# Performance work log

Hardware: AMD Instinct MI355X
Metric: run time of the kernel (lower is better)

The kernel has to match this reference:

```python
import jax, jax.numpy as jnp
import numpy as np

B, S, DM, TD, H, HD = 2, 2048, 1024, 1024, 16, 64


def setup_inputs() -> dict:
    key = jax.random.key(0)
    k1, k2, k3, k4 = jax.random.split(key, 4)
    query = jax.random.normal(k1, (B, S, DM), dtype=jnp.float32)
    # fused QKV projection weight (nn.Linear weight layout: [out, in]) and output proj
    W_in = jax.random.normal(k2, (3 * TD, DM), dtype=jnp.float32) * 0.02
    W_out = jax.random.normal(k3, (DM, TD), dtype=jnp.float32) * 0.02
    # standard RoPE tables, broadcastable against [B, H, S, HD]
    inv_freq = 1.0 / (10000.0 ** (jnp.arange(0, HD, 2, dtype=jnp.float32) / HD))
    t = jnp.arange(S, dtype=jnp.float32)
    freqs = jnp.outer(t, inv_freq)                      # [S, HD/2]
    emb = jnp.concatenate([freqs, freqs], axis=-1)      # [S, HD]
    sin_q = jnp.sin(emb)[None, None]                    # [1,1,S,HD]
    cos_q = jnp.cos(emb)[None, None]
    # padding mask over keys: first length[b] positions valid (>= S/2 so no NaN rows)
    lengths = jax.random.randint(k4, (B,), S // 2, S + 1)
    attn_mask = jnp.arange(S)[None, :] < lengths[:, None]  # [B, S] bool
    return {"query": query, "W_in": W_in, "W_out": W_out,
            "sin_q": sin_q, "cos_q": cos_q, "attn_mask": attn_mask}


def _rotate_half(x):
    x1, x2 = jnp.split(x, 2, axis=-1)
    return jnp.concatenate([-x2, x1], axis=-1)


def reference(query, W_in, W_out, sin_q, cos_q, attn_mask):
    # fused QKV projection (proj_in, bias=False)
    qkv = query @ W_in.T                                # [B, S, 3*TD]
    q, k, v = jnp.split(qkv, 3, axis=-1)
    to_heads = lambda x: x.reshape(B, S, H, HD).transpose(0, 2, 1, 3)  # [B,H,S,HD]
    q, k, v = to_heads(q), to_heads(k), to_heads(v)
    # RoPE (prefix = 0 since sin covers full sequence)
    q = q * cos_q + _rotate_half(q) * sin_q
    k = k * cos_q + _rotate_half(k) * sin_q
    # SDPA with padding-mask bias + causal mask
    scale = 1.0 / jnp.sqrt(jnp.float32(HD))
    scores = jnp.einsum('bhqd,bhkd->bhqk', q, k) * scale  # [B,H,S,S]
    causal = jnp.arange(S)[:, None] >= jnp.arange(S)[None, :]  # [S, S]
    mask = attn_mask[:, None, None, :] & causal[None, None]    # [B,1,S,S]
    scores = jnp.where(mask, scores, -jnp.inf)
    attn = jax.nn.softmax(scores, axis=-1)
    out = jnp.einsum('bhqk,bhkd->bhqd', attn, v)        # [B,H,S,HD]
    out = out.transpose(0, 2, 1, 3).reshape(B, S, TD)
    return out @ W_out.T                                 # [B, S, DM]
```

## Files before the change

kernel.cpp:

```cpp
#include <hip/hip_runtime.h>
#include <hip/hip_bf16.h>

#define B_ 2
#define S_ 2048
#define DM_ 1024
#define TD_ 1024
#define H_ 16
#define HD_ 64

using bf16 = __hip_bfloat16;
typedef __attribute__((ext_vector_type(8))) short s8v;
typedef __attribute__((ext_vector_type(4))) float f4v;

__device__ __forceinline__ f4v mfma_bf16(s8v a, s8v b, f4v c) {
    return __builtin_amdgcn_mfma_f32_16x16x32_bf16(a, b, c, 0, 0, 0);
}

__device__ __forceinline__ unsigned cvt_pk_bf16(float a, float b) {
    unsigned r;
    asm("v_cvt_pk_bf16_f32 %0, %1, %2" : "=v"(r) : "v"(a), "v"(b));
    return r;
}
__device__ __forceinline__ int2 pack4bf(float a, float b, float c, float d) {
    int2 r;
    r.x = (int)cvt_pk_bf16(a, b);
    r.y = (int)cvt_pk_bf16(c, d);
    return r;
}

__device__ __forceinline__ bool detect_f32(const unsigned int* __restrict__ cosw) {
    return (cosw[0] & 0xFFFFu) == 0u;
}

__device__ __forceinline__ void gload_lds16(const bf16* g, void* l) {
    __builtin_amdgcn_global_load_lds(
        (const __attribute__((address_space(1))) unsigned int*)(const void*)g,
        (__attribute__((address_space(3))) unsigned int*)l,
        16, 0, 0);
}

#define NQ_  (B_ * S_ * DM_)
#define NWI_ (3 * TD_ * DM_)
#define NWO_ (DM_ * TD_)
#define NCVT_BLOCKS ((NQ_ + NWI_ + NWO_) / 2048)

__global__ __launch_bounds__(256)
void prep_all(const void* __restrict__ q, const void* __restrict__ wi,
              const void* __restrict__ wo, bf16* __restrict__ dst,
              const void* __restrict__ mask, int* __restrict__ lengths,
              const unsigned int* __restrict__ cosw) {
    const int bid = blockIdx.x;
    if (bid < NCVT_BLOCKS) {
        const bool f32 = detect_f32(cosw);
        int i = (bid * 256 + threadIdx.x) * 8;
        const void* src; int off;
        if (i < NQ_)              { src = q;  off = i; }
        else if (i < NQ_ + NWI_)  { src = wi; off = i - NQ_; }
        else                      { src = wo; off = i - NQ_ - NWI_; }
        if (f32) {
            const float* p = (const float*)src + off;
            float4 x = *reinterpret_cast<const float4*>(p);
            float4 y = *reinterpret_cast<const float4*>(p + 4);
            union { unsigned u[4]; int4 v; } t;
            t.u[0] = cvt_pk_bf16(x.x, x.y);
            t.u[1] = cvt_pk_bf16(x.z, x.w);
            t.u[2] = cvt_pk_bf16(y.x, y.y);
            t.u[3] = cvt_pk_bf16(y.z, y.w);
            *reinterpret_cast<int4*>(dst + i) = t.v;
        } else {
            *reinterpret_cast<int4*>(dst + i) =
                *reinterpret_cast<const int4*>((const bf16*)src + off);
        }
        return;
    }
    int b = bid - NCVT_BLOCKS;
    unsigned int w0 = ((const unsigned int*)mask)[0];
    int enc;
    if (w0 == 1u) enc = 0;
    else if (w0 == 0x01010101u) enc = 1;
    else if (w0 == 0x3F803F80u) enc = 2;
    else enc = 3;
    int cnt = 0;
    for (int s = threadIdx.x; s < S_; s += 256) {
        int i = b * S_ + s;
        bool v;
        if (enc == 0)      v = ((const int*)mask)[i] != 0;
        else if (enc == 1) v = ((const unsigned char*)mask)[i] != 0;
        else if (enc == 2) v = ((const unsigned short*)mask)[i] != 0;
        else               v = ((const float*)mask)[i] != 0.f;
        cnt += v ? 1 : 0;
    }
    __shared__ int red[256];
    red[threadIdx.x] = cnt;
    __syncthreads();
    for (int off = 128; off > 0; off >>= 1) {
        if (threadIdx.x < off) red[threadIdx.x] += red[threadIdx.x + off];
        __syncthreads();
    }
    if (threadIdx.x == 0) lengths[b] = red[0];
}

__global__ __launch_bounds__(256, 4)
void gemm_out(const bf16* __restrict__ A, const bf16* __restrict__ Bm,
              void* __restrict__ C, int M, int N, int K,
              int c_dyn, const unsigned int* __restrict__ cosw) {
    __shared__ bf16 lds_a[128 * 64];
    __shared__ bf16 lds_b[64 * 64];

    const bool cf32 = c_dyn && detect_f32(cosw);

    const int t = threadIdx.x;
    const int wave = t >> 6, lane = t & 63;
    const int quad = lane >> 4, l16 = lane & 15;
    const int wm = wave >> 1, wn = wave & 1;
    const int bid = blockIdx.x;
    const int c = bid & 7, g = bid >> 3;
    const int m0 = (c * 4 + (g & 3)) * 128;
    const int n0 = (g >> 2) * 64;
    const int wuni = __builtin_amdgcn_readfirstlane(wave);

    f4v acc[4][2];
    #pragma unroll
    for (int i = 0; i < 4; i++)
        #pragma unroll
        for (int j = 0; j < 2; j++)
            acc[i][j] = f4v{0.f, 0.f, 0.f, 0.f};

    for (int k0 = 0; k0 < K; k0 += 64) {
        __syncthreads();
        #pragma unroll
        for (int i = 0; i < 4; i++) {
            int ci = i * 256 + t;
            int row = ci >> 3;
            int csrc = (ci & 7) ^ (row & 7);
            gload_lds16(A + (size_t)(m0 + row) * K + k0 + csrc * 8,
                        (char*)lds_a + i * 4096 + wuni * 1024);
        }
        #pragma unroll
        for (int i = 0; i < 2; i++) {
            int ci = i * 256 + t;
            int row = ci >> 3;
            int csrc = (ci & 7) ^ (row & 7);
            gload_lds16(Bm + (size_t)(n0 + row) * K + k0 + csrc * 8,
                        (char*)lds_b + i * 4096 + wuni * 1024);
        }
        __syncthreads();

        #pragma unroll
        for (int kk = 0; kk < 2; kk++) {
            s8v afr[4], bfr[2];
            #pragma unroll
            for (int mb = 0; mb < 4; mb++) {
                int r = wm * 64 + mb * 16 + l16;
                int ch = (kk * 4 + quad) ^ (l16 & 7);
                afr[mb] = *reinterpret_cast<const s8v*>(&lds_a[r * 64 + ch * 8]);
            }
            #pragma unroll
            for (int nb = 0; nb < 2; nb++) {
                int r = wn * 32 + nb * 16 + l16;
                int ch = (kk * 4 + quad) ^ (l16 & 7);
                bfr[nb] = *reinterpret_cast<const s8v*>(&lds_b[r * 64 + ch * 8]);
            }
            #pragma unroll
            for (int mb = 0; mb < 4; mb++)
                #pragma unroll
                for (int nb = 0; nb < 2; nb++)
                    acc[mb][nb] = mfma_bf16(bfr[nb], afr[mb], acc[mb][nb]);
        }
    }

    #pragma unroll
    for (int mb = 0; mb < 4; mb++) {
        int m = m0 + wm * 64 + mb * 16 + l16;
        #pragma unroll
        for (int nb = 0; nb < 2; nb++) {
            int n = n0 + wn * 32 + nb * 16 + quad * 4;
            f4v v = acc[mb][nb];
            if (cf32) {
                *reinterpret_cast<f4v*>(&((float*)C)[(size_t)m * N + n]) = v;
            } else {
                *reinterpret_cast<int2*>(&((bf16*)C)[(size_t)m * N + n]) =
                    pack4bf(v[0], v[1], v[2], v[3]);
            }
        }
    }
}

__global__ __launch_bounds__(256, 3)
void gemm_qkv(const bf16* __restrict__ A, const bf16* __restrict__ Bm,
              bf16* __restrict__ Qh, bf16* __restrict__ Kt, bf16* __restrict__ Vt,
              const void* __restrict__ sin_t, const void* __restrict__ cos_t) {
    __shared__ bf16 lds_a[128 * 64];
    __shared__ bf16 lds_b[128 * 64];

    const int t = threadIdx.x;
    const int wave = t >> 6, lane = t & 63;
    const int quad = lane >> 4, l16 = lane & 15;
    const int wm = wave >> 1, wn = wave & 1;
    const int bid = blockIdx.x;
    const int c = bid & 7, g = bid >> 3;
    const int m0 = (c * 4 + (g & 3)) * 128;
    const int n0 = (g >> 2) * 128;
    const int wuni = __builtin_amdgcn_readfirstlane(wave);

    f4v acc[4][4];
    #pragma unroll
    for (int i = 0; i < 4; i++)
        #pragma unroll
        for (int j = 0; j < 4; j++)
            acc[i][j] = f4v{0.f, 0.f, 0.f, 0.f};

    for (int k0 = 0; k0 < 1024; k0 += 64) {
        __syncthreads();
        #pragma unroll
        for (int i = 0; i < 4; i++) {
            int ci = i * 256 + t;
            int row = ci >> 3;
            int csrc = (ci & 7) ^ (row & 7);
            gload_lds16(A + (size_t)(m0 + row) * 1024 + k0 + csrc * 8,
                        (char*)lds_a + i * 4096 + wuni * 1024);
            gload_lds16(Bm + (size_t)(n0 + row) * 1024 + k0 + csrc * 8,
                        (char*)lds_b + i * 4096 + wuni * 1024);
        }
        __syncthreads();

        #pragma unroll
        for (int kk = 0; kk < 2; kk++) {
            s8v afr[4], bfr[4];
            #pragma unroll
            for (int mb = 0; mb < 4; mb++) {
                int r = wm * 64 + mb * 16 + l16;
                int ch = (kk * 4 + quad) ^ (l16 & 7);
                afr[mb] = *reinterpret_cast<const s8v*>(&lds_a[r * 64 + ch * 8]);
            }
            #pragma unroll
            for (int nb = 0; nb < 4; nb++) {
                int r = wn * 64 + nb * 16 + l16;
                int ch = (kk * 4 + quad) ^ (l16 & 7);
                bfr[nb] = *reinterpret_cast<const s8v*>(&lds_b[r * 64 + ch * 8]);
            }
            #pragma unroll
            for (int mb = 0; mb < 4; mb++)
                #pragma unroll
                for (int nb = 0; nb < 4; nb++)
                    acc[mb][nb] = mfma_bf16(bfr[nb], afr[mb], acc[mb][nb]);
        }
    }

    const int region = n0 >> 10;
    if (region < 2) {
        const bool f32 = detect_f32((const unsigned int*)cos_t);
        #pragma unroll
        for (int mb = 0; mb < 4; mb++) {
            const int m = m0 + wm * 64 + mb * 16 + l16;
            const int b = m >> 11, s = m & 2047;
            #pragma unroll
            for (int nb = 0; nb < 4; nb++) {
                const int n = n0 + wn * 64 + nb * 16 + quad * 4;
                const int d = n & 63;
                const int h = (n >> 6) & 15;
                const float sgn = (nb < 2) ? -1.f : 1.f;
                f4v v  = acc[mb][nb];
                f4v vp = acc[mb][nb ^ 2];
                float cs[4], sn[4];
                if (f32) {
                    float4 c4 = *reinterpret_cast<const float4*>(
                        (const float*)cos_t + s * 64 + d);
                    float4 s4 = *reinterpret_cast<const float4*>(
                        (const float*)sin_t + s * 64 + d);
                    cs[0] = c4.x; cs[1] = c4.y; cs[2] = c4.z; cs[3] = c4.w;
                    sn[0] = s4.x; sn[1] = s4.y; sn[2] = s4.z; sn[3] = s4.w;
                } else {
                    const bf16* cp = (const bf16*)cos_t + s * 64 + d;
                    const bf16* sp = (const bf16*)sin_t + s * 64 + d;
                    #pragma unroll
                    for (int r = 0; r < 4; r++) {
                        cs[r] = __bfloat162float(cp[r]);
                        sn[r] = __bfloat162float(sp[r]);
                    }
                }
                float y[4];
                #pragma unroll
                for (int r = 0; r < 4; r++)
                    y[r] = v[r] * cs[r] + sgn * vp[r] * sn[r];
                if (region == 0) {
                    size_t o = ((size_t)(b * H_ + h) * S_ + s) * 64 + d;
                    *reinterpret_cast<int2*>(&Qh[o]) =
                        pack4bf(y[0] * 0.180336880f, y[1] * 0.180336880f,
                                y[2] * 0.180336880f, y[3] * 0.180336880f);
                } else {
                    size_t kt = ((size_t)(b * H_ + h) * 32 + (s >> 6)) * 4096;
                    int dp = ((((d >> 3) ^ (s & 7)) << 3) | (d & 7));
                    *reinterpret_cast<int2*>(&Kt[kt + (s & 63) * 64 + dp]) =
                        pack4bf(y[0], y[1], y[2], y[3]);
                }
            }
        }
    } else {
        __syncthreads();
        bf16* half_w = (wm == 0) ? lds_a : lds_b;
        #pragma unroll
        for (int mb = 0; mb < 4; mb++) {
            const int slr = mb * 16 + l16;
            #pragma unroll
            for (int nb = 0; nb < 4; nb++) {
                const int nl = wn * 64 + nb * 16 + quad * 4;
                f4v v = acc[mb][nb];
                int off = (((nl >> 3) ^ (slr & 7)) << 3) | (nl & 7);
                *reinterpret_cast<int2*>(&half_w[slr * 128 + off]) =
                    pack4bf(v[0], v[1], v[2], v[3]);
            }
        }
        __syncthreads();
        const int b  = m0 >> 11;
        const int h0 = (n0 - 2048) >> 6;
        const int r0 = t & 7;
        #pragma unroll
        for (int i = 0; i < 8; i++) {
            int id  = i * 256 + t;
            int kc  = id & 7;
            int d   = (id >> 3) & 63;
            int sbl = (id >> 9) & 1;
            int hh  = id >> 10;
            int cb  = (hh << 3) | (d >> 3);
            const short* half_r = reinterpret_cast<const short*>(
                sbl ? lds_b : lds_a);
            union { short s_[8]; int4 v4; } u;
            #pragma unroll
            for (int j = 0; j < 8; j++) {
                int e   = (j + r0) & 7;
                int slr = kc * 8 + e;
                u.s_[e] = half_r[slr * 128 + (((cb ^ e) << 3) | (d & 7))];
            }
            size_t tb = ((size_t)(b * H_ + h0 + hh) * 32 +
                         ((m0 & 2047) >> 6) + sbl) * 4096;
            *reinterpret_cast<int4*>(&Vt[tb + d * 64 + ((kc ^ (d & 7)) << 3)]) = u.v4;
        }
    }
}

__global__ __launch_bounds__(256)
void attn_fused(const bf16* __restrict__ Qh, const bf16* __restrict__ Kt,
                const bf16* __restrict__ Vt, const int* __restrict__ lengths,
                bf16* __restrict__ out) {
    __shared__ bf16 k_buf[2 * 4096];
    __shared__ bf16 v_buf[2 * 4096];
    __shared__ bf16 lds_p[4 * 16 * 72];

    const int t = threadIdx.x, wave = t >> 6, lane = t & 63;
    const int quad = lane >> 4, l16 = lane & 15;
    const int bid = blockIdx.x;
    const int slot = bid >> 3;
    const int bh = (bid & 7) * 4 + (slot >> 4);
    const int p = slot & 15;
    const int b = bh >> 4, h = bh & 15;

    const size_t hb = (size_t)bh * S_ * 64;
    const bf16* Ktp = Kt + (size_t)bh * 32 * 4096;
    const bf16* Vtp = Vt + (size_t)bh * 32 * 4096;
    const int wuni = __builtin_amdgcn_readfirstlane(wave);
    int len_raw = lengths[b];
    const int len_b = len_raw < 1 ? 1 : (len_raw > S_ ? S_ : len_raw);
    const int nkt_len = (len_b + 63) >> 6;

    s8v ones;
    #pragma unroll
    for (int i = 0; i < 8; i++) ones[i] = (short)0x3F80;

    #pragma unroll
    for (int pass = 0; pass < 2; pass++) {
        const int qb = pass ? (31 - p) : p;
        const int qrow_g = qb * 64 + wave * 16 + l16;
        const int kmax = (qrow_g < len_b - 1) ? qrow_g : (len_b - 1);

        s8v qf[2];
        {
            const bf16* qptr = Qh + hb + (size_t)qrow_g * 64 + quad * 8;
            qf[0] = *reinterpret_cast<const s8v*>(qptr);
            qf[1] = *reinterpret_cast<const s8v*>(qptr + 32);
        }

        f4v o_acc[4];
        #pragma unroll
        for (int a = 0; a < 4; a++) o_acc[a] = f4v{0.f, 0.f, 0.f, 0.f};
        f4v l_acc = f4v{0.f, 0.f, 0.f, 0.f};

        const int nkt = (qb + 1) < nkt_len ? (qb + 1) : nkt_len;

        f4v s_prev[4];
        auto process_tile = [&](int pt, const bf16* vb) {
            const int pbase = pt * 64;
            const bool tail = (pt == qb) || (pbase + 64 > len_b);
            #pragma unroll
            for (int a = 0; a < 4; a++) {
                float e0[4];
                #pragma unroll
                for (int r = 0; r < 4; r++) {
                    float e = __builtin_amdgcn_exp2f(s_prev[a][r]);
                    if (tail) {
                        int key = pbase + a * 16 + quad * 4 + r;
                        e = (key <= kmax) ? e : 0.f;
                    }
                    e0[r] = e;
                }
                *reinterpret_cast<int2*>(
                    &lds_p[(wave * 16 + l16) * 72 + a * 16 + quad * 4]) =
                    pack4bf(e0[0], e0[1], e0[2], e0[3]);
            }
            asm volatile("s_waitcnt lgkmcnt(0)" ::: "memory");
            __builtin_amdgcn_s_setprio(1);
            #pragma unroll
            for (int kk = 0; kk < 2; kk++) {
                s8v pf = *reinterpret_cast<const s8v*>(
                    &lds_p[(wave * 16 + l16) * 72 + kk * 32 + quad * 8]);
                l_acc = mfma_bf16(ones, pf, l_acc);
                #pragma unroll
                for (int a = 0; a < 4; a++) {
                    int ch = (kk * 4 + quad) ^ (l16 & 7);
                    s8v vf = *reinterpret_cast<const s8v*>(
                        &vb[(a * 16 + l16) * 64 + ch * 8]);
                    o_acc[a] = mfma_bf16(vf, pf, o_acc[a]);
                }
            }
            __builtin_amdgcn_s_setprio(0);
        };

        #pragma unroll
        for (int i = 0; i < 2; i++) {
            int ci = i * 256 + t;
            gload_lds16(Ktp + ci * 8, (char*)k_buf + i * 4096 + wuni * 1024);
        }
        __syncthreads();

        for (int kt = 0; kt < nkt; kt++) {
            const int cur = kt & 1;
            {
                const bf16* vst = Vtp + (size_t)kt * 4096;
                #pragma unroll
                for (int i = 0; i < 2; i++) {
                    int ci = i * 256 + t;
                    gload_lds16(vst + ci * 8,
                                (char*)v_buf + cur * 8192 + i * 4096 + wuni * 1024);
                }
            }
            if (kt + 1 < nkt) {
                const bf16* kst = Ktp + (size_t)(kt + 1) * 4096;
                #pragma unroll
                for (int i = 0; i < 2; i++) {
                    int ci = i * 256 + t;
                    gload_lds16(kst + ci * 8,
                                (char*)k_buf + (cur ^ 1) * 8192 + i * 4096 + wuni * 1024);
                }
            }

            const bf16* kb = k_buf + cur * 4096;
            f4v s_acc[4];
            #pragma unroll
            for (int a = 0; a < 4; a++) s_acc[a] = f4v{0.f, 0.f, 0.f, 0.f};
            __builtin_amdgcn_s_setprio(1);
            #pragma unroll
            for (int kk = 0; kk < 2; kk++) {
                #pragma unroll
                for (int a = 0; a < 4; a++) {
                    int ch = (kk * 4 + quad) ^ (l16 & 7);
                    s8v kf = *reinterpret_cast<const s8v*>(
                        &kb[(a * 16 + l16) * 64 + ch * 8]);
                    s_acc[a] = mfma_bf16(kf, qf[kk], s_acc[a]);
                }
            }
            __builtin_amdgcn_s_setprio(0);

            if (kt > 0) process_tile(kt - 1, v_buf + ((kt - 1) & 1) * 4096);

            #pragma unroll
            for (int a = 0; a < 4; a++) s_prev[a] = s_acc[a];

            __syncthreads();
        }
        process_tile(nkt - 1, v_buf + ((nkt - 1) & 1) * 4096);

        float inv_l = 1.f / l_acc[0];
        size_t orow = ((size_t)(b * S_ + qrow_g)) * TD_ + h * 64;
        #pragma unroll
        for (int a = 0; a < 4; a++) {
            *reinterpret_cast<int2*>(&out[orow + a * 16 + quad * 4]) =
                pack4bf(o_acc[a][0] * inv_l, o_acc[a][1] * inv_l,
                        o_acc[a][2] * inv_l, o_acc[a][3] * inv_l);
        }
    }
}

extern "C" void kernel_launch(void* const* d_in, const int* in_sizes, int n_in,
                              void* d_out, int out_size, void* d_ws, size_t ws_size,
                              hipStream_t stream) {
    const void* query = d_in[0];
    const void* W_in  = d_in[1];
    const void* W_out = d_in[2];
    const void* sin_q = d_in[3];
    const void* cos_q = d_in[4];
    const void* mask  = d_in[5];
    const unsigned int* cosw = (const unsigned int*)cos_q;

    const size_t nQ  = NQ_;
    const size_t nWi = NWI_;
    const size_t nWo = NWO_;

    bf16* base = (bf16*)d_ws;
    bf16* attn = base;
    bf16* Vt   = base + (size_t)4096 * 1024;
    bf16* Qh   = base + (size_t)2 * 4096 * 1024;
    bf16* Kt   = Qh + nQ;
    bf16* qbf  = Kt + nQ;
    bf16* wibf = qbf + nQ;
    bf16* wobf = wibf + nWi;
    int* lengths = (int*)(wobf + nWo);

    prep_all<<<NCVT_BLOCKS + B_, 256, 0, stream>>>(
        query, W_in, W_out, qbf, mask, lengths, cosw);

    gemm_qkv<<<768, 256, 0, stream>>>(qbf, wibf, Qh, Kt, Vt, sin_q, cos_q);

    attn_fused<<<512, 256, 0, stream>>>(Qh, Kt, Vt, lengths, attn);

    gemm_out<<<512, 256, 0, stream>>>(attn, wobf, d_out, 4096, 1024, 1024, 1, cosw);
}
```

Baseline: 177.0 us.

## Widen attention blocks to 128 query rows with 8 waves sharing K/V tiles

The attention kernel now uses 512-thread blocks covering 128 query rows, so each K/V tile loaded into LDS is reused by eight waves instead of four. The grid is halved, and each thread issues one async load per tile instead of two. This is meant to halve global/LDS fill traffic per query row. In exchange there is more causal-mask work on the diagonal tiles and fewer, larger blocks, which may reduce occupancy or load balance.

```diff
diff --git a/kernel.cpp b/kernel.cpp
--- a/kernel.cpp
+++ b/kernel.cpp
@@ -339,20 +339,20 @@
     }
 }
 
-__global__ __launch_bounds__(256)
+__global__ __launch_bounds__(512)
 void attn_fused(const bf16* __restrict__ Qh, const bf16* __restrict__ Kt,
                 const bf16* __restrict__ Vt, const int* __restrict__ lengths,
                 bf16* __restrict__ out) {
     __shared__ bf16 k_buf[2 * 4096];
     __shared__ bf16 v_buf[2 * 4096];
-    __shared__ bf16 lds_p[4 * 16 * 72];
+    __shared__ bf16 lds_p[8 * 16 * 72];
 
     const int t = threadIdx.x, wave = t >> 6, lane = t & 63;
     const int quad = lane >> 4, l16 = lane & 15;
     const int bid = blockIdx.x;
     const int slot = bid >> 3;
-    const int bh = (bid & 7) * 4 + (slot >> 4);
-    const int p = slot & 15;
+    const int bh = (bid & 7) * 4 + (slot >> 3);
+    const int p = slot & 7;
     const int b = bh >> 4, h = bh & 15;
 
     const size_t hb = (size_t)bh * S_ * 64;
@@ -369,8 +369,8 @@
 
     #pragma unroll
     for (int pass = 0; pass < 2; pass++) {
-        const int qb = pass ? (31 - p) : p;
-        const int qrow_g = qb * 64 + wave * 16 + l16;
+        const int sb = pass ? (15 - p) : p;
+        const int qrow_g = sb * 128 + wave * 16 + l16;
         const int kmax = (qrow_g < len_b - 1) ? qrow_g : (len_b - 1);
 
         s8v qf[2];
@@ -385,12 +385,13 @@
         for (int a = 0; a < 4; a++) o_acc[a] = f4v{0.f, 0.f, 0.f, 0.f};
         f4v l_acc = f4v{0.f, 0.f, 0.f, 0.f};
 
-        const int nkt = (qb + 1) < nkt_len ? (qb + 1) : nkt_len;
+        const int nkt_c = 2 * sb + 2;
+        const int nkt = nkt_c < nkt_len ? nkt_c : nkt_len;
 
         f4v s_prev[4];
         auto process_tile = [&](int pt, const bf16* vb) {
             const int pbase = pt * 64;
-            const bool tail = (pt == qb) || (pbase + 64 > len_b);
+            const bool tail = (pt >= 2 * sb) || (pbase + 64 > len_b);
             #pragma unroll
             for (int a = 0; a < 4; a++) {
                 float e0[4];
@@ -425,32 +426,16 @@
             __builtin_amdgcn_s_setprio(0);
         };
 
-        #pragma unroll
-        for (int i = 0; i < 2; i++) {
-            int ci = i * 256 + t;
-            gload_lds16(Ktp + ci * 8, (char*)k_buf + i * 4096 + wuni * 1024);
-        }
+        gload_lds16(Ktp + t * 8, (char*)k_buf + wuni * 1024);
         __syncthreads();
 
         for (int kt = 0; kt < nkt; kt++) {
             const int cur = kt & 1;
-            {
-                const bf16* vst = Vtp + (size_t)kt * 4096;
-                #pragma unroll
-                for (int i = 0; i < 2; i++) {
-                    int ci = i * 256 + t;
-                    gload_lds16(vst + ci * 8,
-                                (char*)v_buf + cur * 8192 + i * 4096 + wuni * 1024);
-                }
-            }
+            gload_lds16(Vtp + (size_t)kt * 4096 + t * 8,
+                        (char*)v_buf + cur * 8192 + wuni * 1024);
             if (kt + 1 < nkt) {
-                const bf16* kst = Ktp + (size_t)(kt + 1) * 4096;
-                #pragma unroll
-                for (int i = 0; i < 2; i++) {
-                    int ci = i * 256 + t;
-                    gload_lds16(kst + ci * 8,
-                                (char*)k_buf + (cur ^ 1) * 8192 + i * 4096 + wuni * 1024);
-                }
+                gload_lds16(Ktp + (size_t)(kt + 1) * 4096 + t * 8,
+                            (char*)k_buf + (cur ^ 1) * 8192 + wuni * 1024);
             }
 
             const bf16* kb = k_buf + cur * 4096;
@@ -520,7 +505,7 @@
 
     gemm_qkv<<<768, 256, 0, stream>>>(qbf, wibf, Qh, Kt, Vt, sin_q, cos_q);
 
-    attn_fused<<<512, 256, 0, stream>>>(Qh, Kt, Vt, lengths, attn);
+    attn_fused<<<256, 512, 0, stream>>>(Qh, Kt, Vt, lengths, attn);
 
     gemm_out<<<512, 256, 0, stream>>>(attn, wobf, d_out, 4096, 1024, 1024, 1, cosw);
 }
```

New measurement: 180.5 us (median of 2 runs). 2.0% more time.
